# Performance work log

Hardware: AMD Instinct MI355X
Metric: run time of the kernel (lower is better)

Reference implementation:

```python
import jax, jax.numpy as jnp
import numpy as np

# wav2vec2 feature-extractor conv stack config: (kernel, stride) per layer, 512 channels
CONV_CFG = [(10, 5), (3, 2), (3, 2), (3, 2), (3, 2), (2, 2), (2, 2)]
C = 512
PROJ = 256
HID = 128
NCLS = 5
N_WORDS = 64
B = 8
L = 40000


def _conv1d(h, w, stride):
    # h: [B, Cin, T], w: [Cout, Cin, K]
    return jax.lax.conv_general_dilated(
        h, w, window_strides=(stride,), padding='VALID',
        dimension_numbers=('NCH', 'OIH', 'NCH'))


def setup_inputs() -> dict:
    key = jax.random.key(0)
    ks = jax.random.split(key, 16)
    x = jax.random.normal(ks[0], (B, L), dtype=jnp.float32)
    word_ids = jax.random.randint(ks[1], (B,), 0, N_WORDS)
    convs = {}
    cin = 1
    for i, (k, s) in enumerate(CONV_CFG):
        fan = cin * k
        convs[f'conv{i}'] = jax.random.normal(ks[2 + i], (C, cin, k), dtype=jnp.float32) / np.sqrt(fan)
        cin = C
    gn_scale = jnp.ones((C,), dtype=jnp.float32)
    gn_bias = jnp.zeros((C,), dtype=jnp.float32)
    proj_w = jax.random.normal(ks[9], (PROJ, C), dtype=jnp.float32) / np.sqrt(C)
    proj_b = jnp.zeros((PROJ,), dtype=jnp.float32)
    cls_w1 = jax.random.normal(ks[10], (N_WORDS, PROJ, HID), dtype=jnp.float32) / np.sqrt(PROJ)
    cls_b1 = jnp.zeros((N_WORDS, HID), dtype=jnp.float32)
    cls_w2 = jax.random.normal(ks[11], (N_WORDS, HID, NCLS), dtype=jnp.float32) / np.sqrt(HID)
    cls_b2 = jnp.zeros((N_WORDS, NCLS), dtype=jnp.float32)
    return dict(x=x, word_ids=word_ids, gn_scale=gn_scale, gn_bias=gn_bias,
                proj_w=proj_w, proj_b=proj_b, cls_w1=cls_w1, cls_b1=cls_b1,
                cls_w2=cls_w2, cls_b2=cls_b2, **convs)


def _forward(x, convs, gn_scale, gn_bias, proj_w, proj_b, cls_w1, cls_b1, cls_w2, cls_b2, word_ids):
    h = x[:, None, :]  # [B,1,L]
    for i, (k, s) in enumerate(CONV_CFG):
        h = _conv1d(h, convs[i], s)
        if i == 0:
            # wav2vec2 group-norm: groups == channels -> per-channel norm over time
            mu = jnp.mean(h, axis=-1, keepdims=True)
            var = jnp.var(h, axis=-1, keepdims=True)
            h = (h - mu) * jax.lax.rsqrt(var + 1e-5)
            h = h * gn_scale[None, :, None] + gn_bias[None, :, None]
        h = jax.nn.gelu(h)
    feat = jnp.mean(h, axis=-1)                          # [B, 512] mean-pool over time
    feat = jax.nn.relu(feat @ proj_w.T + proj_b)         # [B, 256] (dropout = identity in eval)
    w1 = cls_w1[word_ids]                                # [B, 256, 128] routed gather
    h1 = jax.nn.relu(jnp.einsum('bd,bdh->bh', feat, w1) + cls_b1[word_ids])
    out = jnp.einsum('bh,bho->bo', h1, cls_w2[word_ids]) + cls_b2[word_ids]  # [B, 5]
    return out


def reference(x, word_ids, gn_scale, gn_bias, proj_w, proj_b, cls_w1, cls_b1, cls_w2, cls_b2,
              conv0, conv1, conv2, conv3, conv4, conv5, conv6):
    convs = [conv0, conv1, conv2, conv3, conv4, conv5, conv6]
    return _forward(x, convs, gn_scale, gn_bias, proj_w, proj_b,
                    cls_w1, cls_b1, cls_w2, cls_b2, word_ids)
```

## Files before the change

### kernel.cpp

```cpp
#include <hip/hip_runtime.h>
#include <hip/hip_bf16.h>

typedef unsigned short u16;
typedef short bf16x8 __attribute__((ext_vector_type(8)));
typedef float f32x4 __attribute__((ext_vector_type(4)));

#define CC 512

constexpr int vmimm(int n) {
    return (n & 0xF) | ((n >> 4) << 14) | (0x7 << 4) | (0xF << 8);
}

__device__ __forceinline__ float gelu_tanh(float x) {
    float x3 = x * x * x;
    float z  = 0.7978845608028654f * (x + 0.044715f * x3);
    float e  = __expf(2.0f * z);
    float th = 1.0f - 2.0f / (e + 1.0f);
    return 0.5f * x * (1.0f + th);
}

__device__ __forceinline__ u16 f2bf(float f) {
    union { float f; unsigned u; } v; v.f = f;
    unsigned r = v.u + 0x7fff + ((v.u >> 16) & 1);
    return (u16)(r >> 16);
}
__device__ __forceinline__ float bf2f(u16 h) {
    union { unsigned u; float f; } v; v.u = ((unsigned)h) << 16; return v.f;
}

__global__ __launch_bounds__(256) void conv0_stats(
    const float* __restrict__ x, const float* __restrict__ w0,
    float* __restrict__ part) {
    const int t0 = blockIdx.x * 64, b = blockIdx.y;
    __shared__ float xs[64 * 5 + 16];
    __shared__ float w0t[10 * 512];
    __shared__ float redS[4][512], redQ[4][512];
    for (int i = threadIdx.x; i < 64 * 5 + 5; i += 256) {
        int gi = t0 * 5 + i;
        xs[i] = (gi < 40000) ? x[b * 40000 + gi] : 0.0f;
    }
    for (int i = threadIdx.x; i < 5120; i += 256) {
        int c = i / 10, j = i - c * 10;
        w0t[j * 512 + c] = w0[i];
    }
    __syncthreads();
    const int lane = threadIdx.x & 63, wv = threadIdx.x >> 6;
    float wr[8][10];
#pragma unroll
    for (int q = 0; q < 8; ++q)
#pragma unroll
        for (int j = 0; j < 10; ++j) wr[q][j] = w0t[j * 512 + lane + 64 * q];
    float sacc[8] = {}, qacc[8] = {};
#pragma unroll
    for (int u = 0; u < 16; ++u) {
        const int tt = wv * 16 + u;
        const int t  = t0 + tt;
        float xv[10];
#pragma unroll
        for (int j = 0; j < 10; ++j) xv[j] = xs[tt * 5 + j];
#pragma unroll
        for (int q = 0; q < 8; ++q) {
            float a = 0.0f;
#pragma unroll
            for (int j = 0; j < 10; ++j) a = fmaf(wr[q][j], xv[j], a);
            if (t < 7999) {
                const float ar = bf2f(f2bf(a));
                sacc[q] += ar; qacc[q] += ar * ar;
            }
        }
    }
#pragma unroll
    for (int q = 0; q < 8; ++q) {
        redS[wv][lane + 64 * q] = sacc[q];
        redQ[wv][lane + 64 * q] = qacc[q];
    }
    __syncthreads();
    float* pp = part + (((size_t)blockIdx.x * 8 + b) * 512) * 2;
#pragma unroll
    for (int half = 0; half < 2; ++half) {
        const int c = half * 256 + threadIdx.x;
        const float s = redS[0][c] + redS[1][c] + redS[2][c] + redS[3][c];
        const float q = redQ[0][c] + redQ[1][c] + redQ[2][c] + redQ[3][c];
        pp[c * 2] = s; pp[c * 2 + 1] = q;
    }
}

__global__ __launch_bounds__(256) void stats_finalizeAB(
    const float* __restrict__ part, const float* __restrict__ gsc,
    const float* __restrict__ gbi, float* __restrict__ Af, float* __restrict__ Bf) {
    const int r4 = threadIdx.x & 63, kg = threadIdx.x >> 6;
    const int row = blockIdx.x * 64 + r4;
    float s = 0.0f, q = 0.0f;
    for (int k = kg; k < 125; k += 4) {
        const float2 v = *(const float2*)(part + ((size_t)k * 4096 + row) * 2);
        s += v.x; q += v.y;
    }
    __shared__ float rs[4][64], rq[4][64];
    rs[kg][r4] = s; rq[kg][r4] = q;
    __syncthreads();
    if (kg == 0) {
        s = rs[0][r4] + rs[1][r4] + rs[2][r4] + rs[3][r4];
        q = rq[0][r4] + rq[1][r4] + rq[2][r4] + rq[3][r4];
        float mean = s / 7999.0f;
        float var  = fmaxf(q / 7999.0f - mean * mean, 0.0f);
        float rstd = rsqrtf(var + 1e-5f);
        const int c = row & (CC - 1);
        float A = rstd * gsc[c];
        Af[row] = A;
        Bf[row] = gbi[c] - mean * A;
    }
}

__global__ __launch_bounds__(256) void conv0_norm(
    const float* __restrict__ x, const float* __restrict__ w0,
    const float* __restrict__ Af, const float* __restrict__ Bf,
    u16* __restrict__ actG) {
    const int t0 = blockIdx.x * 64, b = blockIdx.y;
    __shared__ float xs[64 * 5 + 16];
    __shared__ float w0t[10 * 512];
    for (int i = threadIdx.x; i < 64 * 5 + 5; i += 256) {
        int gi = t0 * 5 + i;
        xs[i] = (gi < 40000) ? x[b * 40000 + gi] : 0.0f;
    }
    for (int i = threadIdx.x; i < 5120; i += 256) {
        int c = i / 10, j = i - c * 10;
        w0t[j * 512 + c] = w0[i];
    }
    __syncthreads();
    const int lane = threadIdx.x & 63, wv = threadIdx.x >> 6;
    float wr[8][10];
    float Ar[8], Br[8];
#pragma unroll
    for (int q = 0; q < 8; ++q) {
        const int c = lane + 64 * q;
#pragma unroll
        for (int j = 0; j < 10; ++j) wr[q][j] = w0t[j * 512 + c];
        Ar[q] = Af[b * 512 + c];
        Br[q] = Bf[b * 512 + c];
    }
    u16* ob = actG + ((size_t)b * 8320 + t0 + wv * 16) * 512 + lane;
#pragma unroll
    for (int u = 0; u < 16; ++u) {
        const int tt = wv * 16 + u;
        const int t  = t0 + tt;
        float xv[10];
#pragma unroll
        for (int j = 0; j < 10; ++j) xv[j] = xs[tt * 5 + j];
#pragma unroll
        for (int q = 0; q < 8; ++q) {
            float a = 0.0f;
#pragma unroll
            for (int j = 0; j < 10; ++j) a = fmaf(wr[q][j], xv[j], a);
            u16 outv = 0;
            if (t < 7999) {
                const float ar = bf2f(f2bf(a));
                outv = f2bf(gelu_tanh(fmaf(ar, Ar[q], Br[q])));
            }
            ob[(size_t)u * 512 + 64 * q] = outv;
        }
    }
}

template <int K, int NL>
struct WtBatch { const float* src[NL]; u16* dst[NL]; };

template <int K, int NL>
__global__ __launch_bounds__(256) void wt_transform(WtBatch<K, NL> a) {
    constexpr int WROW = 32 * K + 8;
    const int cit = blockIdx.x, cob = blockIdx.y, l = blockIdx.z;
    const float* w = a.src[l];
    u16* dst = a.dst[l] + ((size_t)(cob * 16 + cit)) * 128 * WROW;
    for (int idx = threadIdx.x; idx < 128 * WROW; idx += 256) {
        const int co = idx / WROW, e = idx - co * WROW;
        u16 hi = 0;
        if (e < 32 * K) {
            const int j = e >> 5, ci = e & 31;
            hi = f2bf(w[((size_t)(cob * 128 + co) * 512 + cit * 32 + ci) * K + j]);
        }
        dst[idx] = hi;
    }
}

template <int K, int TT>
__global__ __launch_bounds__(256, 2) void conv_mfma(
    const u16* __restrict__ act, int capIn,
    const u16* __restrict__ wt,
    u16* __restrict__ outAct, int capOut, int tbShift) {
    constexpr int WROW = 32 * K + 8;
    constexpr int XH   = TT + 8;
    constexpr int TF   = TT / 32;
    constexpr int TXC  = XH * 8;
    constexpr int CPX  = TXC / 4;
    constexpr int NIX  = (CPX + 63) / 64;
    constexpr int XLAST = CPX - (NIX - 1) * 64;
    constexpr int TWC  = 128 * WROW / 8;
    constexpr int CPW  = TWC / 4;
    constexpr int NIW  = (CPW + 63) / 64;
    constexpr int WLAST = CPW - (NIW - 1) * 64;

    __shared__ __align__(16) u16 Xs[2][XH * 64];
    __shared__ __align__(16) u16 Ws[128 * WROW];

    const int tid  = threadIdx.x;
    const int lane = tid & 63;
    const int wv   = tid >> 6;
    const int wco  = wv >> 1, wtt = wv & 1;
    const int l15  = lane & 15, l16 = lane >> 4;

    const int flat = blockIdx.x;
    const int xcd  = flat & 7, cob = (flat >> 3) & 3;
    const int G    = xcd + (flat >> 5) * 8;
    const int t_b  = G & ((1 << tbShift) - 1);
    const int b    = G >> tbShift;
    const int t0   = t_b * TT;
    const int x0   = t0 * 2;

    const char* abase = (const char*)(act + (size_t)b * capIn * 512);
    const u16*  wbase = wt + (size_t)cob * (16 * 128 * WROW);

    const char* xsA[NIX]; const char* xsB[NIX]; int xdst[NIX];
#pragma unroll
    for (int i = 0; i < NIX; ++i) {
        const int c  = wv * CPX + i * 64 + lane;
        const int xh = c >> 3;
        const int li = ((c & 7) * 16) ^ ((xh & 7) << 4);
        const int xx = min(x0 + 2 * xh + (li >> 6), capIn - 1);
        xsA[i] = abase + (size_t)xx * 1024 + (li & 63);
        xsB[i] = xsA[i] + 64;
        xdst[i] = (wv * CPX + i * 64) * 16;
    }
    const char* wsrc[NIW]; int wdst[NIW];
#pragma unroll
    for (int i = 0; i < NIW; ++i) {
        wsrc[i] = (const char*)wbase + (size_t)(wv * CPW + i * 64 + lane) * 16;
        wdst[i] = (wv * CPW + i * 64) * 16;
    }

    auto stageX = [&](const char* (&xs)[NIX], u16* xb) {
#pragma unroll
        for (int i = 0; i < NIX; ++i)
            if (i < NIX - 1 || lane < XLAST)
                __builtin_amdgcn_global_load_lds(
                    (const __attribute__((address_space(1))) void*)xs[i],
                    (__attribute__((address_space(3))) void*)((char*)xb + xdst[i]),
                    16, 0, 0);
#pragma unroll
        for (int i = 0; i < NIX; ++i) xs[i] += 128;
    };
    auto stageW = [&]() {
#pragma unroll
        for (int i = 0; i < NIW; ++i)
            if (i < NIW - 1 || lane < WLAST)
                __builtin_amdgcn_global_load_lds(
                    (const __attribute__((address_space(1))) void*)wsrc[i],
                    (__attribute__((address_space(3))) void*)((char*)&Ws[0] + wdst[i]),
                    16, 0, 0);
#pragma unroll
        for (int i = 0; i < NIW; ++i) wsrc[i] += WROW * 256;
    };

    int xoff[K][TF];
    int woff[K][4];
#pragma unroll
    for (int j = 0; j < K; ++j) {
#pragma unroll
        for (int tf = 0; tf < TF; ++tf) {
            const int tl = wtt * (TT / 2) + tf * 16 + l15;
            const int xl = 2 * tl + j;
            const int xh = xl >> 1, p = xl & 1;
            xoff[j][tf] = xh * 128 + ((p * 64 + l16 * 16) ^ ((xh & 7) << 4));
        }
#pragma unroll
        for (int cf = 0; cf < 4; ++cf)
            woff[j][cf] = ((wco * 64 + cf * 16 + l15) * WROW + j * 32 + l16 * 8) * 2;
    }

    f32x4 acc[4][TF] = {};

    stageX(xsA, &Xs[0][0]);
    stageX(xsB, &Xs[1][0]);
    stageW();
    __syncthreads();

    auto body = [&](int cit, u16* xb, const char* (&xset)[NIX]) {
        bf16x8 xr[K][TF], wr[K][4];
#pragma unroll
        for (int j = 0; j < K; ++j) {
#pragma unroll
            for (int tf = 0; tf < TF; ++tf)
                xr[j][tf] = *(const bf16x8*)((const char*)xb + xoff[j][tf]);
#pragma unroll
            for (int cf = 0; cf < 4; ++cf)
                wr[j][cf] = *(const bf16x8*)((const char*)&Ws[0] + woff[j][cf]);
        }
        asm volatile("s_waitcnt lgkmcnt(0)" ::: "memory");
        __builtin_amdgcn_s_barrier();
        if (cit < 15) stageW();
        if (cit < 14) stageX(xset, xb);
#pragma unroll
        for (int j = 0; j < K; ++j)
#pragma unroll
            for (int cf = 0; cf < 4; ++cf)
#pragma unroll
                for (int tf = 0; tf < TF; ++tf)
                    acc[cf][tf] = __builtin_amdgcn_mfma_f32_16x16x32_bf16(
                        wr[j][cf], xr[j][tf], acc[cf][tf], 0, 0, 0);
        if (cit < 14) {
            __builtin_amdgcn_s_waitcnt(vmimm(NIX));
            __builtin_amdgcn_s_barrier();
        } else if (cit == 14) {
            __builtin_amdgcn_s_waitcnt(vmimm(0));
            __builtin_amdgcn_s_barrier();
        }
    };

#pragma unroll 1
    for (int c2 = 0; c2 < 16; c2 += 2) {
        body(c2,     &Xs[0][0], xsA);
        body(c2 + 1, &Xs[1][0], xsB);
    }

    u16* ob = outAct + (size_t)b * capOut * 512;
#pragma unroll
    for (int cf = 0; cf < 4; ++cf) {
#pragma unroll
        for (int tf = 0; tf < TF; ++tf) {
            const int tG  = t0 + wtt * (TT / 2) + tf * 16 + l15;
            const int coG = cob * 128 + wco * 64 + cf * 16 + l16 * 4;
            union { u16 s[4]; uint2 v; } pk;
#pragma unroll
            for (int r = 0; r < 4; ++r)
                pk.s[r] = f2bf(gelu_tanh(acc[cf][tf][r]));
            *(uint2*)(ob + (size_t)tG * 512 + coG) = pk.v;
        }
    }
}

__global__ __launch_bounds__(512) void feat_proj_kernel(
    const u16* __restrict__ act, int cap,
    const float* __restrict__ pw, const float* __restrict__ pb,
    float* __restrict__ pfeat) {
    const int b = blockIdx.x;
    __shared__ float fs[8][512];
    __shared__ float feat[CC];
    const int c8 = (threadIdx.x & 63) * 8;
    const int tg = threadIdx.x >> 6;
    float s[8] = {};
    for (int t = tg; t < 124; t += 8) {
        union { u16 u[8]; uint4 v; } in;
        in.v = *(const uint4*)(act + ((size_t)b * cap + t) * 512 + c8);
#pragma unroll
        for (int e = 0; e < 8; ++e) s[e] += bf2f(in.u[e]);
    }
#pragma unroll
    for (int e = 0; e < 8; ++e) fs[tg][c8 + e] = s[e];
    __syncthreads();
    {
        const int c = threadIdx.x;
        if (c < 512) {
            float acc = 0.0f;
#pragma unroll
            for (int g = 0; g < 8; ++g) acc += fs[g][c];
            feat[c] = acc * (1.0f / 124.0f);
        }
    }
    __syncthreads();
    if (threadIdx.x < 256) {
        const int j = threadIdx.x;
        const float* wr = pw + (size_t)j * CC;
        float acc = pb[j];
        for (int cc = 0; cc < CC; ++cc) acc = fmaf(feat[cc], wr[cc], acc);
        pfeat[b * 256 + j] = fmaxf(acc, 0.0f);
    }
}

__global__ __launch_bounds__(128) void cls_kernel(
    const float* __restrict__ pfeat, const int* __restrict__ wid,
    const float* __restrict__ w1, const float* __restrict__ b1,
    const float* __restrict__ w2, const float* __restrict__ b2,
    float* __restrict__ out) {
    const int b = blockIdx.x;
    const int id = wid[b];
    __shared__ float pf[256], h1[128];
    for (int d = threadIdx.x; d < 256; d += 128) pf[d] = pfeat[b * 256 + d];
    __syncthreads();
    {
        const int hh = threadIdx.x;
        const float* w1p = w1 + (size_t)id * 256 * 128;
        float s = b1[id * 128 + hh];
        for (int d = 0; d < 256; ++d) s = fmaf(pf[d], w1p[d * 128 + hh], s);
        h1[hh] = fmaxf(s, 0.0f);
    }
    __syncthreads();
    if (threadIdx.x < 5) {
        const float* w2p = w2 + (size_t)id * 128 * 5;
        float s = b2[id * 5 + threadIdx.x];
        for (int hh = 0; hh < 128; ++hh) s = fmaf(h1[hh], w2p[hh * 5 + threadIdx.x], s);
        out[b * 5 + threadIdx.x] = s;
    }
}

extern "C" void kernel_launch(void* const* d_in, const int* in_sizes, int n_in,
                              void* d_out, int out_size, void* d_ws, size_t ws_size,
                              hipStream_t stream) {
    const float* x   = (const float*)d_in[0];
    const int*   wid = (const int*)d_in[1];
    const float* gsc = (const float*)d_in[2];
    const float* gbi = (const float*)d_in[3];
    const float* pw  = (const float*)d_in[4];
    const float* pb  = (const float*)d_in[5];
    const float* w1  = (const float*)d_in[6];
    const float* b1  = (const float*)d_in[7];
    const float* w2  = (const float*)d_in[8];
    const float* b2  = (const float*)d_in[9];
    const float* cw[7];
    for (int i = 0; i < 7; ++i) cw[i] = (const float*)d_in[10 + i];

    char* ws = (char*)d_ws;
    const size_t SZ_ACTG = (size_t)8 * 8320 * 512 * 2;
    const size_t SZ_P    = (size_t)8 * 4224 * 512 * 2;
    const size_t SZ_Q    = (size_t)8 * 2176 * 512 * 2;
    u16* actG = (u16*)ws;
    u16* bufP = (u16*)(ws + SZ_ACTG);
    u16* bufQ = (u16*)(ws + SZ_ACTG + SZ_P);
    size_t off = SZ_ACTG + SZ_P + SZ_Q;
    u16* wtbuf[7];
    for (int i = 1; i <= 4; ++i) { wtbuf[i] = (u16*)(ws + off); off += (size_t)4 * 16 * 128 * 104 * 2; }
    for (int i = 5; i <= 6; ++i) { wtbuf[i] = (u16*)(ws + off); off += (size_t)4 * 16 * 128 * 72 * 2; }
    off = (off + 255) & ~(size_t)255;
    float* statsPart = (float*)(ws + off); off += (size_t)125 * 8 * 512 * 2 * 4;
    float* Af        = (float*)(ws + off); off += 4096 * 4;
    float* Bf        = (float*)(ws + off); off += 4096 * 4;
    float* pfeat     = (float*)(ws + off); off += 8 * 256 * 4;

    conv0_stats<<<dim3(125, 8), 256, 0, stream>>>(x, cw[0], statsPart);
    stats_finalizeAB<<<dim3(64), 256, 0, stream>>>(statsPart, gsc, gbi, Af, Bf);
    conv0_norm<<<dim3(125, 8), 256, 0, stream>>>(x, cw[0], Af, Bf, actG);

    {
        WtBatch<3, 4> a;
        for (int i = 0; i < 4; ++i) { a.src[i] = cw[1 + i]; a.dst[i] = wtbuf[1 + i]; }
        wt_transform<3, 4><<<dim3(16, 4, 4), 256, 0, stream>>>(a);
        WtBatch<2, 2> c;
        for (int i = 0; i < 2; ++i) { c.src[i] = cw[5 + i]; c.dst[i] = wtbuf[5 + i]; }
        wt_transform<2, 2><<<dim3(16, 4, 2), 256, 0, stream>>>(c);
    }

    conv_mfma<3, 128><<<dim3(32 * 32), 256, 0, stream>>>(actG, 8320, wtbuf[1], bufP, 4224, 5);
    conv_mfma<3, 128><<<dim3(16 * 32), 256, 0, stream>>>(bufP, 4224, wtbuf[2], bufQ, 2176, 4);
    conv_mfma<3,  64><<<dim3(16 * 32), 256, 0, stream>>>(bufQ, 2176, wtbuf[3], bufP, 4224, 4);
    conv_mfma<3,  64><<<dim3( 8 * 32), 256, 0, stream>>>(bufP, 4224, wtbuf[4], bufQ, 2176, 3);
    conv_mfma<2,  64><<<dim3( 4 * 32), 256, 0, stream>>>(bufQ, 2176, wtbuf[5], bufP, 4224, 2);
    conv_mfma<2,  64><<<dim3( 2 * 32), 256, 0, stream>>>(bufP, 4224, wtbuf[6], bufQ, 2176, 1);

    feat_proj_kernel<<<dim3(8), 512, 0, stream>>>(bufQ, 2176, pw, pb, pfeat);
    cls_kernel<<<dim3(8), 128, 0, stream>>>(pfeat, wid, w1, b1, w2, b2, (float*)d_out);
}
```

Baseline: 308.1 us.

## Load conv weights directly into registers instead of staging through LDS

Drops the shared-memory weight buffer. Each wave now loads its weight fragments straight from global memory into registers, prefetching the next input-channel tile's weights right after the MFMAs that consume each tap. The waitcnt threshold is adjusted to count these extra outstanding loads. This removes LDS traffic and a staging step for weights and frees LDS for occupancy, but raises register pressure and duplicates global or L2 weight reads across the waves that share a weight block.

```diff
diff --git a/kernel.cpp b/kernel.cpp
--- a/kernel.cpp
+++ b/kernel.cpp
@@ -187,19 +187,17 @@
     const u16* __restrict__ wt,
     u16* __restrict__ outAct, int capOut, int tbShift) {
     constexpr int WROW = 32 * K + 8;
+    constexpr int PLANE = 128 * WROW;
     constexpr int XH   = TT + 8;
     constexpr int TF   = TT / 32;
     constexpr int TXC  = XH * 8;
     constexpr int CPX  = TXC / 4;
     constexpr int NIX  = (CPX + 63) / 64;
     constexpr int XLAST = CPX - (NIX - 1) * 64;
-    constexpr int TWC  = 128 * WROW / 8;
-    constexpr int CPW  = TWC / 4;
-    constexpr int NIW  = (CPW + 63) / 64;
-    constexpr int WLAST = CPW - (NIW - 1) * 64;
+    constexpr int WREF = K * 4;
+    constexpr int VM_MAIN = NIX + 2 * WREF;
 
     __shared__ __align__(16) u16 Xs[2][XH * 64];
-    __shared__ __align__(16) u16 Ws[128 * WROW];
 
     const int tid  = threadIdx.x;
     const int lane = tid & 63;
@@ -216,7 +214,7 @@
     const int x0   = t0 * 2;
 
     const char* abase = (const char*)(act + (size_t)b * capIn * 512);
-    const u16*  wbase = wt + (size_t)cob * (16 * 128 * WROW);
+    const u16*  wbase = wt + (size_t)cob * (16 * PLANE);
 
     const char* xsA[NIX]; const char* xsB[NIX]; int xdst[NIX];
 #pragma unroll
@@ -229,12 +227,6 @@
         xsB[i] = xsA[i] + 64;
         xdst[i] = (wv * CPX + i * 64) * 16;
     }
-    const char* wsrc[NIW]; int wdst[NIW];
-#pragma unroll
-    for (int i = 0; i < NIW; ++i) {
-        wsrc[i] = (const char*)wbase + (size_t)(wv * CPW + i * 64 + lane) * 16;
-        wdst[i] = (wv * CPW + i * 64) * 16;
-    }
 
     auto stageX = [&](const char* (&xs)[NIX], u16* xb) {
 #pragma unroll
@@ -247,20 +239,9 @@
 #pragma unroll
         for (int i = 0; i < NIX; ++i) xs[i] += 128;
     };
-    auto stageW = [&]() {
-#pragma unroll
-        for (int i = 0; i < NIW; ++i)
-            if (i < NIW - 1 || lane < WLAST)
-                __builtin_amdgcn_global_load_lds(
-                    (const __attribute__((address_space(1))) void*)wsrc[i],
-                    (__attribute__((address_space(3))) void*)((char*)&Ws[0] + wdst[i]),
-                    16, 0, 0);
-#pragma unroll
-        for (int i = 0; i < NIW; ++i) wsrc[i] += WROW * 256;
-    };
 
     int xoff[K][TF];
-    int woff[K][4];
+    int woffB[K][4];
 #pragma unroll
     for (int j = 0; j < K; ++j) {
 #pragma unroll
@@ -272,41 +253,50 @@
         }
 #pragma unroll
         for (int cf = 0; cf < 4; ++cf)
-            woff[j][cf] = ((wco * 64 + cf * 16 + l15) * WROW + j * 32 + l16 * 8) * 2;
+            woffB[j][cf] = ((wco * 64 + cf * 16 + l15) * WROW + j * 32 + l16 * 8) * 2;
     }
 
     f32x4 acc[4][TF] = {};
+    bf16x8 wr[K][4];
 
     stageX(xsA, &Xs[0][0]);
     stageX(xsB, &Xs[1][0]);
-    stageW();
+    const char* wNext = (const char*)wbase;
+#pragma unroll
+    for (int j = 0; j < K; ++j)
+#pragma unroll
+        for (int cf = 0; cf < 4; ++cf)
+            wr[j][cf] = *(const bf16x8*)(wNext + woffB[j][cf]);
+    wNext += PLANE * 2;
     __syncthreads();
 
     auto body = [&](int cit, u16* xb, const char* (&xset)[NIX]) {
-        bf16x8 xr[K][TF], wr[K][4];
-#pragma unroll
-        for (int j = 0; j < K; ++j) {
+        bf16x8 xr[K][TF];
+#pragma unroll
+        for (int j = 0; j < K; ++j)
 #pragma unroll
             for (int tf = 0; tf < TF; ++tf)
                 xr[j][tf] = *(const bf16x8*)((const char*)xb + xoff[j][tf]);
-#pragma unroll
-            for (int cf = 0; cf < 4; ++cf)
-                wr[j][cf] = *(const bf16x8*)((const char*)&Ws[0] + woff[j][cf]);
-        }
         asm volatile("s_waitcnt lgkmcnt(0)" ::: "memory");
         __builtin_amdgcn_s_barrier();
-        if (cit < 15) stageW();
         if (cit < 14) stageX(xset, xb);
 #pragma unroll
-        for (int j = 0; j < K; ++j)
+        for (int j = 0; j < K; ++j) {
 #pragma unroll
             for (int cf = 0; cf < 4; ++cf)
 #pragma unroll
                 for (int tf = 0; tf < TF; ++tf)
                     acc[cf][tf] = __builtin_amdgcn_mfma_f32_16x16x32_bf16(
                         wr[j][cf], xr[j][tf], acc[cf][tf], 0, 0, 0);
+            if (cit < 15) {
+#pragma unroll
+                for (int cf = 0; cf < 4; ++cf)
+                    wr[j][cf] = *(const bf16x8*)(wNext + woffB[j][cf]);
+            }
+        }
+        wNext += PLANE * 2;
         if (cit < 14) {
-            __builtin_amdgcn_s_waitcnt(vmimm(NIX));
+            __builtin_amdgcn_s_waitcnt(vmimm(VM_MAIN));
             __builtin_amdgcn_s_barrier();
         } else if (cit == 14) {
             __builtin_amdgcn_s_waitcnt(vmimm(0));
```

New measurement: 374.4 us. +21.5%, slower.
